# Performance work log

Hardware: AMD Instinct MI355X
Metric: run time of the kernel (lower is better)

The kernel has to match this reference:

```python
import jax, jax.numpy as jnp
import numpy as np

SIGMA = 1e-4          # flow-matching sigma (init kwarg)
OT_EPS = 0.01         # entropic regularization for the batched OT solve
OT_ITERS = 100        # Sinkhorn iterations


def _sinkhorn_log(M, eps, iters):
    """Log-domain Sinkhorn with uniform marginals. M: [B,N,N] cost (max-normalized).
    Returns log coupling log(pi): [B,N,N]. GPU-native batched replacement for the
    per-sample pot.emd network-simplex solve in the original."""
    B, N, _ = M.shape
    loga = -jnp.log(jnp.asarray(N, M.dtype))  # uniform marginal log prob
    f = jnp.zeros((B, N), M.dtype)
    g = jnp.zeros((B, N), M.dtype)

    def body(carry, _):
        f, g = carry
        g = eps * (loga - jax.scipy.special.logsumexp((f[:, :, None] - M) / eps, axis=1))
        f = eps * (loga - jax.scipy.special.logsumexp((g[:, None, :] - M) / eps, axis=2))
        return (f, g), None

    (f, g), _ = jax.lax.scan(body, (f, g), None, length=iters)
    return (f[:, :, None] + g[:, None, :] - M) / eps


def setup_inputs() -> dict:
    key = jax.random.key(0)
    ks = jax.random.split(key, 8)
    B, N, F, H = 512, 150, 3, 512
    x = jax.random.normal(ks[0], (B, N, F), jnp.float32)
    mask = jnp.ones((B, N, 1), jnp.float32)
    t = jax.random.uniform(ks[1], (B,), jnp.float32)
    x0_noise = jax.random.normal(ks[2], (B, N, F), jnp.float32)
    eps_noise = jax.random.normal(ks[3], (B, N, F), jnp.float32)
    W1 = 0.05 * jax.random.normal(ks[4], (F + 1, H), jnp.float32)
    b1 = jnp.zeros((H,), jnp.float32)
    W2 = 0.05 * jax.random.normal(ks[5], (H, F), jnp.float32)
    b2 = jnp.zeros((F,), jnp.float32)
    return {"x": x, "mask": mask, "t": t, "x0_noise": x0_noise,
            "eps_noise": eps_noise, "W1": W1, "b1": b1, "W2": W2, "b2": b2}


def reference(x, mask, t, x0_noise, eps_noise, W1, b1, W2, b2):
    B, N, F = x.shape
    x0, x1 = x0_noise, x                        # noise source / data target

    # squared pairwise distances, per-batch max-normalized (as in the torch code)
    M = jnp.sum((x0[:, :, None, :] - x1[:, None, :, :]) ** 2, axis=-1)  # [B,N,N]
    M = M / jnp.max(M, axis=(1, 2), keepdims=True)
    M = jax.lax.stop_gradient(M)                # original detaches M before emd

    logpi = _sinkhorn_log(M, OT_EPS, OT_ITERS)  # [B,N,N] log OT coupling

    # Sample N i.i.d. (i, j) pairs per batch from the flattened coupling.
    # Row marginal of pi is uniform -> i ~ Uniform(N), j ~ pi[i, :] / (1/N).
    key = jax.random.key(42)
    ki, kj = jax.random.split(key)
    i = jax.random.randint(ki, (B, N), 0, N)                       # [B,N]
    rows = jnp.take_along_axis(logpi, i[:, :, None], axis=1)       # [B,N,N]
    j = jax.random.categorical(kj, rows, axis=-1)                  # [B,N]

    x0s = jnp.take_along_axis(x0, i[:, :, None], axis=1)           # [B,N,F]
    x1s = jnp.take_along_axis(x1, j[:, :, None], axis=1)           # [B,N,F]
    mask_ot = jnp.take_along_axis(mask, j[:, :, None], axis=1)     # [B,N,1]

    tb = t[:, None, None]                                          # [B,1,1]
    mu_t = x0s * tb + x1s * (1.0 - tb)
    y = mu_t + SIGMA * eps_noise
    ut = (x0s - x1s) * mask_ot

    # stand-in flow network: per-particle MLP on [y, t]
    h = jnp.concatenate([y, jnp.broadcast_to(tb, (B, N, 1))], axis=-1)  # [B,N,F+1]
    h = jax.nn.gelu(h @ W1 + b1)
    vt = (h @ W2 + b2) * mask_ot

    return jnp.mean((vt - ut) ** 2)
```

## Files before the change

kernel.cpp:

```cpp
#include <hip/hip_runtime.h>
#include <cstdint>

#define B_ 512
#define N_ 150
#define NT 640
#define NTS 768
#define PPS 152
#define C1f 144.26950408889634f
#define LN2f 0.69314718055994531f
#define SIGMAf 1.0e-4f
#define INV_N (1.0f/150.0f)

#define EXP2R(x) __builtin_amdgcn_exp2f(x)
#define LOG2R(x) __builtin_amdgcn_logf(x)

#define DPPF(v, c) __int_as_float(__builtin_amdgcn_update_dpp( \
    __float_as_int(v), __float_as_int(v), (c), 0xF, 0xF, false))
#define RED4_ADD(v)  { v = v + DPPF(v, 0xB1); v = v + DPPF(v, 0x4E); }

#define REP10(X) X(0) X(1) X(2) X(3) X(4) X(5) X(6) X(7) X(8) X(9)

__host__ __device__ __forceinline__ void tf2x32(uint32_t k0, uint32_t k1,
                                                uint32_t x0, uint32_t x1,
                                                uint32_t& o0, uint32_t& o1) {
  uint32_t ks2 = k0 ^ k1 ^ 0x1BD11BDAu;
  x0 += k0; x1 += k1;
#define TFR(r) { x0 += x1; x1 = (x1 << r) | (x1 >> (32 - r)); x1 ^= x0; }
  TFR(13) TFR(15) TFR(26) TFR(6)
  x0 += k1;  x1 += ks2 + 1u;
  TFR(17) TFR(29) TFR(16) TFR(24)
  x0 += ks2; x1 += k0 + 2u;
  TFR(13) TFR(15) TFR(26) TFR(6)
  x0 += k0;  x1 += k1 + 3u;
  TFR(17) TFR(29) TFR(16) TFR(24)
  x0 += k1;  x1 += ks2 + 4u;
  TFR(13) TFR(15) TFR(26) TFR(6)
  x0 += ks2; x1 += k0 + 5u;
#undef TFR
  o0 = x0; o1 = x1;
}

__device__ __forceinline__ uint32_t jax_bits(uint32_t k0, uint32_t k1, uint32_t p) {
  uint32_t a, b; tf2x32(k0, k1, 0u, p, a, b);
  return a ^ b;
}

__global__ __launch_bounds__(NT, 5) void cfm_ot_kernel(
    const float* __restrict__ x1g, const float* __restrict__ x0g,
    float* __restrict__ pp)
{
  __shared__ float x1L[480], x0L[480];
  __shared__ __align__(16) float colp[16 * 164];
  __shared__ __align__(16) float rowqT[10 * 162];
  __shared__ __align__(16) float vhat[160];
  __shared__ __align__(16) float uhatP[16 * 12];
  __shared__ float red[16];
  float4* colp4 = (float4*)colp;
  float4* vhat4 = (float4*)vhat;

  const int b    = blockIdx.x;
  const int tid  = threadIdx.x;
  const int lane = tid & 63;
  const int wid  = tid >> 6;
  const int rg   = tid / 40;
  const int cg   = tid - rg * 40;
  const int q    = tid & 3;
  const int cgq  = cg >> 2;
  const int rbase = rg * 10;
  const int cbase = cg * 4;

  if (tid < 480) {
    x1L[tid] = (tid < 450) ? x1g[b * 450 + tid] : 0.f;
    x0L[tid] = (tid < 450) ? x0g[b * 450 + tid] : 0.f;
  }
  if (tid < 192) uhatP[tid] = 1.0f;
  __syncthreads();

  float4 kt0, kt1, kt2, kt3, kt4, kt5, kt6, kt7, kt8, kt9;
  float lmax = 0.f;
  {
    const float c0 = x1L[cbase * 3 + 0], c1 = x1L[cbase * 3 + 1], c2 = x1L[cbase * 3 + 2];
    const float d0 = x1L[cbase * 3 + 3], d1 = x1L[cbase * 3 + 4], d2 = x1L[cbase * 3 + 5];
    const float e0 = x1L[cbase * 3 + 6], e1 = x1L[cbase * 3 + 7], e2 = x1L[cbase * 3 + 8];
    const float f0 = x1L[cbase * 3 + 9], f1 = x1L[cbase * 3 + 10], f2 = x1L[cbase * 3 + 11];
#define DIST(r) { \
    const int row = rbase + r; \
    const float rx = x0L[row * 3 + 0], ry = x0L[row * 3 + 1], rz = x0L[row * 3 + 2]; \
    float dx, dy, dz, d; \
    dx = rx - c0; dy = ry - c1; dz = rz - c2; \
    d = fmaf(dz, dz, fmaf(dy, dy, dx * dx)); \
    kt##r.x = (row < N_ && cbase + 0 < N_) ? d : 0.f; \
    dx = rx - d0; dy = ry - d1; dz = rz - d2; \
    d = fmaf(dz, dz, fmaf(dy, dy, dx * dx)); \
    kt##r.y = (row < N_ && cbase + 1 < N_) ? d : 0.f; \
    dx = rx - e0; dy = ry - e1; dz = rz - e2; \
    d = fmaf(dz, dz, fmaf(dy, dy, dx * dx)); \
    kt##r.z = (row < N_ && cbase + 2 < N_) ? d : 0.f; \
    dx = rx - f0; dy = ry - f1; dz = rz - f2; \
    d = fmaf(dz, dz, fmaf(dy, dy, dx * dx)); \
    kt##r.w = (row < N_ && cbase + 3 < N_) ? d : 0.f; \
    lmax = fmaxf(lmax, fmaxf(fmaxf(kt##r.x, kt##r.y), fmaxf(kt##r.z, kt##r.w))); }
    REP10(DIST)
#undef DIST
  }
  #pragma unroll
  for (int off = 1; off < 64; off <<= 1) lmax = fmaxf(lmax, __shfl_xor(lmax, off));
  if (lane == 0) red[wid] = lmax;
  __syncthreads();
  if (tid == 0) {
    float m = red[0];
    #pragma unroll
    for (int w = 1; w < 10; ++w) m = fmaxf(m, red[w]);
    red[15] = -C1f / m;
  }
  __syncthreads();
  const float nsc = red[15];

#define TOK(r) { \
    const int row = rbase + r; \
    kt##r.x = (row < N_ && cbase + 0 < N_) ? EXP2R(nsc * kt##r.x) : 0.f; \
    kt##r.y = (row < N_ && cbase + 1 < N_) ? EXP2R(nsc * kt##r.y) : 0.f; \
    kt##r.z = (row < N_ && cbase + 2 < N_) ? EXP2R(nsc * kt##r.z) : 0.f; \
    kt##r.w = (row < N_ && cbase + 3 < N_) ? EXP2R(nsc * kt##r.w) : 0.f; }
  REP10(TOK)
#undef TOK

  for (int it = 0; it < 100; ++it) {
    {
      const float4 ua = *(const float4*)&uhatP[rg * 12];
      const float4 ub = *(const float4*)&uhatP[rg * 12 + 4];
      const float2 uc = *(const float2*)&uhatP[rg * 12 + 8];
      float4 p4 = make_float4(0.f, 0.f, 0.f, 0.f);
#define COLA(k, uu) { \
      p4.x = fmaf(kt##k.x, uu, p4.x); \
      p4.y = fmaf(kt##k.y, uu, p4.y); \
      p4.z = fmaf(kt##k.z, uu, p4.z); \
      p4.w = fmaf(kt##k.w, uu, p4.w); }
      COLA(0, ua.x) COLA(1, ua.y) COLA(2, ua.z) COLA(3, ua.w)
      COLA(4, ub.x) COLA(5, ub.y) COLA(6, ub.z) COLA(7, ub.w)
      COLA(8, uc.x) COLA(9, uc.y)
#undef COLA
      colp4[rg * 41 + cg] = p4;
    }
    __syncthreads();
    if (tid < 160) {
      float s = 0.f;
      #pragma unroll
      for (int k = 0; k < 16; ++k) s += colp[k * 164 + tid];
      vhat[tid] = __builtin_amdgcn_rcpf(fmaxf(s, 1e-37f)) * INV_N;
    }
    __syncthreads();
    {
      const float4 vv = vhat4[cg];
#define ROWB(k) \
      float rp##k = kt##k.x * vv.x; \
      rp##k = fmaf(kt##k.y, vv.y, rp##k); \
      rp##k = fmaf(kt##k.z, vv.z, rp##k); \
      rp##k = fmaf(kt##k.w, vv.w, rp##k); \
      RED4_ADD(rp##k)
      REP10(ROWB)
#undef ROWB
      if (q == 0) {
        const int rb2 = cgq * 162 + rbase;
        *(float2*)&rowqT[rb2 + 0] = make_float2(rp0, rp1);
        *(float2*)&rowqT[rb2 + 2] = make_float2(rp2, rp3);
        *(float2*)&rowqT[rb2 + 4] = make_float2(rp4, rp5);
        *(float2*)&rowqT[rb2 + 6] = make_float2(rp6, rp7);
        *(float2*)&rowqT[rb2 + 8] = make_float2(rp8, rp9);
      }
    }
    __syncthreads();
    if (tid < 160) {
      float s = 0.f;
      #pragma unroll
      for (int u = 0; u < 10; ++u) s += rowqT[u * 162 + tid];
      const float uh = __builtin_amdgcn_rcpf(fmaxf(s, 1e-37f)) * INV_N;
      const int g = tid / 10;
      uhatP[g * 12 + (tid - g * 10)] = uh;
    }
    __syncthreads();
  }

  if (tid < N_) pp[b * PPS + tid] = LOG2R(vhat[tid]);
  if (tid == 0) pp[b * PPS + 150] = nsc;
}

__global__ __launch_bounds__(NTS) void cfm_sample_kernel(
    const float* __restrict__ x1g, const float* __restrict__ maskg,
    const float* __restrict__ tg, const float* __restrict__ x0g,
    const float* __restrict__ epsg,
    const float* __restrict__ W1, const float* __restrict__ b1,
    const float* __restrict__ W2, const float* __restrict__ b2,
    const float* __restrict__ pp, float* __restrict__ partials,
    uint32_t kj0, uint32_t kj1, uint32_t k1r0, uint32_t k1r1,
    uint32_t k2r0, uint32_t k2r1)
{
  __shared__ float x1L[450], x0L[450], psiS[152], mskS[152];
  __shared__ float yu[150 * 9];
  __shared__ float aP[4 * 160 * 3];
  __shared__ float lossS[160];
  __shared__ int   iselS[152];

  const int b    = blockIdx.x;
  const int tid  = threadIdx.x;
  const int lane = tid & 63;
  const int wid  = tid >> 6;

  if (tid < 450) {
    x1L[tid] = x1g[b * 450 + tid];
    x0L[tid] = x0g[b * 450 + tid];
  }
  if (tid < N_) {
    psiS[tid] = pp[b * PPS + tid];
    mskS[tid] = maskg[b * 150 + tid];
    const uint32_t p = (uint32_t)(b * N_ + tid);
    const uint32_t hb = jax_bits(k1r0, k1r1, p);
    const uint32_t lb = jax_bits(k2r0, k2r1, p);
    iselS[tid] = (int)(((hb % 150u) * 46u + (lb % 150u)) % 150u);
  }
  const float nsc = pp[b * PPS + 150];
  const float tb  = tg[b];
  __syncthreads();

  for (int n = wid; n < N_; n += 12) {
    const uint32_t p = (uint32_t)(b * N_ + n);
    const int isel = iselS[n];
    const float xi0 = x0L[isel * 3 + 0], xi1 = x0L[isel * 3 + 1], xi2 = x0L[isel * 3 + 2];

    float best = -1e30f; int bestk = 0x7fffffff;
    #pragma unroll
    for (int c2 = 0; c2 < 3; ++c2) {
      const int k = lane + 64 * c2;
      if (k < N_) {
        const uint32_t bits = jax_bits(kj0, kj1, p * 150u + (uint32_t)k);
        float u = __uint_as_float((bits >> 9) | 0x3F800000u) - 1.0f;
        u = fmaxf(u, 1.17549435e-38f);
        const float nlu = -LN2f * LOG2R(u);
        const float g = -LN2f * LOG2R(nlu);
        const float dx = xi0 - x1L[k * 3 + 0];
        const float dy = xi1 - x1L[k * 3 + 1];
        const float dz = xi2 - x1L[k * 3 + 2];
        const float d2 = fmaf(dz, dz, fmaf(dy, dy, dx * dx));
        const float val = fmaf(psiS[k] + nsc * d2, LN2f, g);
        if (val > best || (val == best && k < bestk)) { best = val; bestk = k; }
      }
    }
    #pragma unroll
    for (int off = 1; off < 64; off <<= 1) {
      const float ov = __shfl_xor(best, off);
      const int   ok = __shfl_xor(bestk, off);
      if (ov > best || (ov == best && ok < bestk)) { best = ov; bestk = ok; }
    }
    if (lane == 0) {
      const int j = bestk;
      const float mot = mskS[j];
      const float q0 = x1L[j * 3 + 0], q1 = x1L[j * 3 + 1], q2 = x1L[j * 3 + 2];
      const float omt = 1.f - tb;
      yu[n * 9 + 0] = xi0 * tb + q0 * omt + SIGMAf * epsg[b * 450 + n * 3 + 0];
      yu[n * 9 + 1] = xi1 * tb + q1 * omt + SIGMAf * epsg[b * 450 + n * 3 + 1];
      yu[n * 9 + 2] = xi2 * tb + q2 * omt + SIGMAf * epsg[b * 450 + n * 3 + 2];
      yu[n * 9 + 3] = (xi0 - q0) * mot;
      yu[n * 9 + 4] = (xi1 - q1) * mot;
      yu[n * 9 + 5] = (xi2 - q2) * mot;
      yu[n * 9 + 6] = mot;
    }
  }
  __syncthreads();

  {
    const int qtr = wid / 3;
    const int sw  = wid - qtr * 3;
    const int s   = sw * 64 + lane;
    if (s < N_) {
      const float y0 = yu[s * 9 + 0], y1 = yu[s * 9 + 1], y2 = yu[s * 9 + 2];
      float a0 = 0.f, a1 = 0.f, a2 = 0.f;
      const int h0 = qtr * 128;
      #pragma unroll 4
      for (int i = 0; i < 128; ++i) {
        const int hd = h0 + i;
        float z = b1[hd];
        z = fmaf(y0, W1[hd],        z);
        z = fmaf(y1, W1[512 + hd],  z);
        z = fmaf(y2, W1[1024 + hd], z);
        z = fmaf(tb, W1[1536 + hd], z);
        const float zc = fmaf(0.044715f * z, z * z, z);
        const float e2 = EXP2R(-2.3022082062161855f * zc);
        const float ge = z * __builtin_amdgcn_rcpf(1.f + e2);
        a0 = fmaf(ge, W2[hd * 3 + 0], a0);
        a1 = fmaf(ge, W2[hd * 3 + 1], a1);
        a2 = fmaf(ge, W2[hd * 3 + 2], a2);
      }
      aP[(qtr * 160 + s) * 3 + 0] = a0;
      aP[(qtr * 160 + s) * 3 + 1] = a1;
      aP[(qtr * 160 + s) * 3 + 2] = a2;
    }
  }
  __syncthreads();

  if (tid < N_) {
    float a0 = aP[(0 * 160 + tid) * 3 + 0] + aP[(1 * 160 + tid) * 3 + 0]
             + aP[(2 * 160 + tid) * 3 + 0] + aP[(3 * 160 + tid) * 3 + 0];
    float a1 = aP[(0 * 160 + tid) * 3 + 1] + aP[(1 * 160 + tid) * 3 + 1]
             + aP[(2 * 160 + tid) * 3 + 1] + aP[(3 * 160 + tid) * 3 + 1];
    float a2 = aP[(0 * 160 + tid) * 3 + 2] + aP[(1 * 160 + tid) * 3 + 2]
             + aP[(2 * 160 + tid) * 3 + 2] + aP[(3 * 160 + tid) * 3 + 2];
    const float mot = yu[tid * 9 + 6];
    const float v0 = (a0 + b2[0]) * mot;
    const float v1 = (a1 + b2[1]) * mot;
    const float v2 = (a2 + b2[2]) * mot;
    const float d0 = v0 - yu[tid * 9 + 3];
    const float d1 = v1 - yu[tid * 9 + 4];
    const float d2 = v2 - yu[tid * 9 + 5];
    lossS[tid] = fmaf(d2, d2, fmaf(d1, d1, d0 * d0));
  }
  __syncthreads();

  if (wid == 0) {
    float s = 0.f;
    #pragma unroll
    for (int k = 0; k < 3; ++k) {
      const int idx = lane + 64 * k;
      if (idx < N_) s += lossS[idx];
    }
    #pragma unroll
    for (int off = 1; off < 64; off <<= 1) s += __shfl_xor(s, off);
    if (lane == 0) partials[b] = s;
  }
}

__global__ void cfm_reduce_kernel(const float* __restrict__ partials,
                                  float* __restrict__ out) {
  const int tid = threadIdx.x;
  float s = 0.f;
  #pragma unroll
  for (int q = 0; q < 8; ++q) s += partials[tid + 64 * q];
  #pragma unroll
  for (int off = 1; off < 64; off <<= 1) s += __shfl_xor(s, off);
  if (tid == 0) out[0] = s * (1.0f / 230400.0f);
}

extern "C" void kernel_launch(void* const* d_in, const int* in_sizes, int n_in,
                              void* d_out, int out_size, void* d_ws, size_t ws_size,
                              hipStream_t stream) {
  (void)in_sizes; (void)n_in; (void)out_size; (void)ws_size;
  const float* x    = (const float*)d_in[0];
  const float* mask = (const float*)d_in[1];
  const float* t    = (const float*)d_in[2];
  const float* x0n  = (const float*)d_in[3];
  const float* epsn = (const float*)d_in[4];
  const float* W1   = (const float*)d_in[5];
  const float* b1   = (const float*)d_in[6];
  const float* W2   = (const float*)d_in[7];
  const float* b2   = (const float*)d_in[8];
  float* out = (float*)d_out;

  float* pp       = (float*)d_ws;
  float* partials = pp + B_ * PPS;

  uint32_t ki0, ki1, kj0, kj1, k1r0, k1r1, k2r0, k2r1;
  tf2x32(0u, 42u, 0u, 0u, ki0, ki1);
  tf2x32(0u, 42u, 0u, 1u, kj0, kj1);
  tf2x32(ki0, ki1, 0u, 0u, k1r0, k1r1);
  tf2x32(ki0, ki1, 0u, 1u, k2r0, k2r1);

  cfm_ot_kernel<<<B_, NT, 0, stream>>>(x, x0n, pp);
  cfm_sample_kernel<<<B_, NTS, 0, stream>>>(x, mask, t, x0n, epsn, W1, b1, W2, b2,
                                            pp, partials,
                                            kj0, kj1, k1r0, k1r1, k2r0, k2r1);
  cfm_reduce_kernel<<<1, 64, 0, stream>>>(partials, out);
}
```

Measured before the change: 253.2 us.

## Fuse Sinkhorn OT kernel with sampling/MLP loss kernel into one launch

Merges the OT potential kernel and the sampling plus MLP loss kernel into a single 640-thread kernel per batch. The potentials, normalizer and particle data stay in shared memory instead of going through a global workspace. This removes a kernel launch, the global round trip, and the reload of x0/x1. The sampling and MLP stages now use 10 waves instead of 12, with the hidden dimension split into two halves of 256. This leaves some waves idle in the MLP stage and adds shared-memory pressure that could limit occupancy under the 5-blocks launch bound.

Result: no change. 250.4 us (median of 2 runs) (-1.1%).

```diff
diff --git a/kernel.cpp b/kernel.cpp
--- a/kernel.cpp
+++ b/kernel.cpp
@@ -4,8 +4,6 @@
 #define B_ 512
 #define N_ 150
 #define NT 640
-#define NTS 768
-#define PPS 152
 #define C1f 144.26950408889634f
 #define LN2f 0.69314718055994531f
 #define SIGMAf 1.0e-4f
@@ -45,9 +43,15 @@
   return a ^ b;
 }
 
-__global__ __launch_bounds__(NT, 5) void cfm_ot_kernel(
-    const float* __restrict__ x1g, const float* __restrict__ x0g,
-    float* __restrict__ pp)
+__global__ __launch_bounds__(NT, 5) void cfm_fused_kernel(
+    const float* __restrict__ x1g, const float* __restrict__ maskg,
+    const float* __restrict__ tg, const float* __restrict__ x0g,
+    const float* __restrict__ epsg,
+    const float* __restrict__ W1, const float* __restrict__ b1,
+    const float* __restrict__ W2, const float* __restrict__ b2,
+    float* __restrict__ partials,
+    uint32_t kj0, uint32_t kj1, uint32_t k1r0, uint32_t k1r1,
+    uint32_t k2r0, uint32_t k2r1)
 {
   __shared__ float x1L[480], x0L[480];
   __shared__ __align__(16) float colp[16 * 164];
@@ -55,6 +59,11 @@
   __shared__ __align__(16) float vhat[160];
   __shared__ __align__(16) float uhatP[16 * 12];
   __shared__ float red[16];
+  __shared__ float psiS[152], mskS[152];
+  __shared__ float yu[150 * 9];
+  __shared__ float aP[2 * 160 * 3];
+  __shared__ float lossS[160];
+  __shared__ int   iselS[152];
   float4* colp4 = (float4*)colp;
   float4* vhat4 = (float4*)vhat;
 
@@ -181,48 +190,18 @@
     __syncthreads();
   }
 
-  if (tid < N_) pp[b * PPS + tid] = LOG2R(vhat[tid]);
-  if (tid == 0) pp[b * PPS + 150] = nsc;
-}
-
-__global__ __launch_bounds__(NTS) void cfm_sample_kernel(
-    const float* __restrict__ x1g, const float* __restrict__ maskg,
-    const float* __restrict__ tg, const float* __restrict__ x0g,
-    const float* __restrict__ epsg,
-    const float* __restrict__ W1, const float* __restrict__ b1,
-    const float* __restrict__ W2, const float* __restrict__ b2,
-    const float* __restrict__ pp, float* __restrict__ partials,
-    uint32_t kj0, uint32_t kj1, uint32_t k1r0, uint32_t k1r1,
-    uint32_t k2r0, uint32_t k2r1)
-{
-  __shared__ float x1L[450], x0L[450], psiS[152], mskS[152];
-  __shared__ float yu[150 * 9];
-  __shared__ float aP[4 * 160 * 3];
-  __shared__ float lossS[160];
-  __shared__ int   iselS[152];
-
-  const int b    = blockIdx.x;
-  const int tid  = threadIdx.x;
-  const int lane = tid & 63;
-  const int wid  = tid >> 6;
-
-  if (tid < 450) {
-    x1L[tid] = x1g[b * 450 + tid];
-    x0L[tid] = x0g[b * 450 + tid];
-  }
   if (tid < N_) {
-    psiS[tid] = pp[b * PPS + tid];
+    psiS[tid] = LOG2R(vhat[tid]);
     mskS[tid] = maskg[b * 150 + tid];
     const uint32_t p = (uint32_t)(b * N_ + tid);
     const uint32_t hb = jax_bits(k1r0, k1r1, p);
     const uint32_t lb = jax_bits(k2r0, k2r1, p);
     iselS[tid] = (int)(((hb % 150u) * 46u + (lb % 150u)) % 150u);
   }
-  const float nsc = pp[b * PPS + 150];
-  const float tb  = tg[b];
-  __syncthreads();
-
-  for (int n = wid; n < N_; n += 12) {
+  const float tb = tg[b];
+  __syncthreads();
+
+  for (int n = wid; n < N_; n += 10) {
     const uint32_t p = (uint32_t)(b * N_ + n);
     const int isel = iselS[n];
     const float xi0 = x0L[isel * 3 + 0], xi1 = x0L[isel * 3 + 1], xi2 = x0L[isel * 3 + 2];
@@ -268,15 +247,15 @@
   __syncthreads();
 
   {
-    const int qtr = wid / 3;
-    const int sw  = wid - qtr * 3;
-    const int s   = sw * 64 + lane;
-    if (s < N_) {
+    const int h  = wid / 5;
+    const int sw = wid - h * 5;
+    const int s  = sw * 64 + lane;
+    if (sw < 3 && s < N_) {
       const float y0 = yu[s * 9 + 0], y1 = yu[s * 9 + 1], y2 = yu[s * 9 + 2];
       float a0 = 0.f, a1 = 0.f, a2 = 0.f;
-      const int h0 = qtr * 128;
+      const int h0 = h * 256;
       #pragma unroll 4
-      for (int i = 0; i < 128; ++i) {
+      for (int i = 0; i < 256; ++i) {
         const int hd = h0 + i;
         float z = b1[hd];
         z = fmaf(y0, W1[hd],        z);
@@ -290,20 +269,17 @@
         a1 = fmaf(ge, W2[hd * 3 + 1], a1);
         a2 = fmaf(ge, W2[hd * 3 + 2], a2);
       }
-      aP[(qtr * 160 + s) * 3 + 0] = a0;
-      aP[(qtr * 160 + s) * 3 + 1] = a1;
-      aP[(qtr * 160 + s) * 3 + 2] = a2;
+      aP[(h * 160 + s) * 3 + 0] = a0;
+      aP[(h * 160 + s) * 3 + 1] = a1;
+      aP[(h * 160 + s) * 3 + 2] = a2;
     }
   }
   __syncthreads();
 
   if (tid < N_) {
-    float a0 = aP[(0 * 160 + tid) * 3 + 0] + aP[(1 * 160 + tid) * 3 + 0]
-             + aP[(2 * 160 + tid) * 3 + 0] + aP[(3 * 160 + tid) * 3 + 0];
-    float a1 = aP[(0 * 160 + tid) * 3 + 1] + aP[(1 * 160 + tid) * 3 + 1]
-             + aP[(2 * 160 + tid) * 3 + 1] + aP[(3 * 160 + tid) * 3 + 1];
-    float a2 = aP[(0 * 160 + tid) * 3 + 2] + aP[(1 * 160 + tid) * 3 + 2]
-             + aP[(2 * 160 + tid) * 3 + 2] + aP[(3 * 160 + tid) * 3 + 2];
+    const float a0 = aP[tid * 3 + 0] + aP[(160 + tid) * 3 + 0];
+    const float a1 = aP[tid * 3 + 1] + aP[(160 + tid) * 3 + 1];
+    const float a2 = aP[tid * 3 + 2] + aP[(160 + tid) * 3 + 2];
     const float mot = yu[tid * 9 + 6];
     const float v0 = (a0 + b2[0]) * mot;
     const float v1 = (a1 + b2[1]) * mot;
@@ -353,9 +329,7 @@
   const float* W2   = (const float*)d_in[7];
   const float* b2   = (const float*)d_in[8];
   float* out = (float*)d_out;
-
-  float* pp       = (float*)d_ws;
-  float* partials = pp + B_ * PPS;
+  float* partials = (float*)d_ws;
 
   uint32_t ki0, ki1, kj0, kj1, k1r0, k1r1, k2r0, k2r1;
   tf2x32(0u, 42u, 0u, 0u, ki0, ki1);
@@ -363,9 +337,8 @@
   tf2x32(ki0, ki1, 0u, 0u, k1r0, k1r1);
   tf2x32(ki0, ki1, 0u, 1u, k2r0, k2r1);
 
-  cfm_ot_kernel<<<B_, NT, 0, stream>>>(x, x0n, pp);
-  cfm_sample_kernel<<<B_, NTS, 0, stream>>>(x, mask, t, x0n, epsn, W1, b1, W2, b2,
-                                            pp, partials,
-                                            kj0, kj1, k1r0, k1r1, k2r0, k2r1);
+  cfm_fused_kernel<<<B_, NT, 0, stream>>>(x, mask, t, x0n, epsn, W1, b1, W2, b2,
+                                          partials,
+                                          kj0, kj1, k1r0, k1r1, k2r0, k2r1);
   cfm_reduce_kernel<<<1, 64, 0, stream>>>(partials, out);
 }
```
